# Kernel tuning notes

Hardware: AMD Instinct MI355X
Metric: run time of the kernel (lower is better)

## Reference

```python
import jax, jax.numpy as jnp
import numpy as np

STRIDE = 16
A = 9
PRE_NMS_TOP_N = 6000
POST_NMS_TOP_N = 300
NMS_THRESH = 0.7
MIN_SIZE = 16
H, W = 128, 192


def _generate_anchors(base_size=16, ratios=(0.5, 1.0, 2.0), scales=(8, 16, 32)):
    base = np.array([0, 0, base_size - 1, base_size - 1], dtype=np.float64)
    w = base[2] - base[0] + 1
    h = base[3] - base[1] + 1
    x_ctr = base[0] + 0.5 * (w - 1)
    y_ctr = base[1] + 0.5 * (h - 1)
    size = w * h
    ratios = np.array(ratios)
    ws = np.round(np.sqrt(size / ratios))
    hs = np.round(ws * ratios)
    ratio_anchors = np.stack([x_ctr - 0.5 * (ws - 1), y_ctr - 0.5 * (hs - 1),
                              x_ctr + 0.5 * (ws - 1), y_ctr + 0.5 * (hs - 1)], axis=1)
    out = []
    scales = np.array(scales)
    for a in ratio_anchors:
        aw = a[2] - a[0] + 1
        ah = a[3] - a[1] + 1
        xc = a[0] + 0.5 * (aw - 1)
        yc = a[1] + 0.5 * (ah - 1)
        ws2 = aw * scales
        hs2 = ah * scales
        out.append(np.stack([xc - 0.5 * (ws2 - 1), yc - 0.5 * (hs2 - 1),
                             xc + 0.5 * (ws2 - 1), yc + 0.5 * (hs2 - 1)], axis=1))
    return np.concatenate(out, axis=0).astype(np.float32)  # [9,4]


def setup_inputs() -> dict:
    key = jax.random.key(0)
    k1, k2 = jax.random.split(key)
    scores = jax.random.uniform(k1, (1, 2 * A, H, W), dtype=jnp.float32)
    bbox_deltas = 0.1 * jax.random.normal(k2, (1, 4 * A, H, W), dtype=jnp.float32)
    im_info = jnp.array([[H * STRIDE, W * STRIDE, 1.0]], dtype=jnp.float32)
    return {"scores": scores, "bbox_deltas": bbox_deltas, "im_info": im_info}


def _proposal_forward(scores, bbox_deltas, im_info):
    anchors_base = jnp.asarray(_generate_anchors())  # [A,4]
    sc = scores[:, A:, :, :]                          # fg scores [1,A,H,W]
    h, w = sc.shape[-2], sc.shape[-1]
    shift_x = (jnp.arange(w) * STRIDE).astype(sc.dtype)
    shift_y = (jnp.arange(h) * STRIDE).astype(sc.dtype)
    sy, sx = jnp.meshgrid(shift_y, shift_x, indexing='ij')
    shifts = jnp.stack([sx.ravel(), sy.ravel(), sx.ravel(), sy.ravel()], axis=1)  # [K,4]
    anchors = (anchors_base[None, :, :] + shifts[:, None, :]).reshape(-1, 4)      # [K*A,4]

    deltas = bbox_deltas.transpose(0, 2, 3, 1).reshape(-1, 4)
    deltas = jnp.concatenate([deltas[:, :2], jnp.clip(deltas[:, 2:], -10.0, 10.0)], axis=1)
    sc = sc.transpose(0, 2, 3, 1).reshape(-1)  # [K*A]

    widths = anchors[:, 2] - anchors[:, 0] + 1.0
    heights = anchors[:, 3] - anchors[:, 1] + 1.0
    ctr_x = anchors[:, 0] + 0.5 * widths
    ctr_y = anchors[:, 1] + 0.5 * heights
    dx, dy, dw, dh = deltas[:, 0], deltas[:, 1], deltas[:, 2], deltas[:, 3]
    pcx = dx * widths + ctr_x
    pcy = dy * heights + ctr_y
    pw = jnp.exp(dw) * widths
    ph = jnp.exp(dh) * heights
    x1 = pcx - 0.5 * pw
    y1 = pcy - 0.5 * ph
    x2 = pcx + 0.5 * pw
    y2 = pcy + 0.5 * ph

    info = im_info[0]
    x1 = jnp.clip(x1, 0.0, info[1] - 1.0)
    x2 = jnp.clip(x2, 0.0, info[1] - 1.0)
    y1 = jnp.clip(y1, 0.0, info[0] - 1.0)
    y2 = jnp.clip(y2, 0.0, info[0] - 1.0)
    proposals = jnp.stack([x1, y1, x2, y2], axis=1)

    # filter_boxes: mask (instead of dropping) boxes smaller than min_size*scale
    min_sz = MIN_SIZE * info[2]
    valid = ((x2 - x1 + 1.0) >= min_sz) & ((y2 - y1 + 1.0) >= min_sz)
    masked = jnp.where(valid, sc, -jnp.inf)

    # sort desc + pre_nms_topN
    top_scores, top_idx = jax.lax.top_k(masked, PRE_NMS_TOP_N)
    boxes = proposals[top_idx]               # [PRE,4], score-descending
    tvalid = top_scores > -jnp.inf

    # pairwise IoU (torchvision convention)
    area = (boxes[:, 2] - boxes[:, 0]) * (boxes[:, 3] - boxes[:, 1])
    lt = jnp.maximum(boxes[:, None, :2], boxes[None, :, :2])
    rb = jnp.minimum(boxes[:, None, 2:], boxes[None, :, 2:])
    wh = jnp.clip(rb - lt, 0.0)
    inter = wh[..., 0] * wh[..., 1]
    iou = inter / (area[:, None] + area[None, :] - inter)  # [PRE,PRE]

    # greedy NMS over score-sorted boxes
    n = PRE_NMS_TOP_N
    def step(keep, x):
        iou_col, v, i = x
        suppressed = jnp.any(keep & (iou_col > NMS_THRESH))
        k = v & jnp.logical_not(suppressed)
        keep = keep.at[i].set(k)
        return keep, k
    keep, _ = jax.lax.scan(step, jnp.zeros((n,), dtype=bool),
                           (iou.T, tvalid, jnp.arange(n)))

    # kept boxes first (stable => score order preserved), take post_nms_topN
    order = jnp.argsort(jnp.logical_not(keep).astype(jnp.int32), stable=True)[:POST_NMS_TOP_N]
    kept = keep[order]
    out_boxes = jnp.where(kept[:, None], boxes[order], 0.0)
    output = jnp.concatenate(
        [jnp.zeros((POST_NMS_TOP_N, 1), out_boxes.dtype), out_boxes], axis=1)
    return output  # [POST,5]: (batch_idx=0, x1,y1,x2,y2); rows beyond kept count are zero


def reference(scores, bbox_deltas, im_info):
    return _proposal_forward(scores, bbox_deltas, im_info)
```

## Files before the change

### kernel.cpp

```cpp
#include <hip/hip_runtime.h>

#define N_ANCH 221184
#define HW     24576
#define Wd     192
#define AA     9
#define TOPN   6000
#define POSTN  300
#define CAND_CAP 8192
#define NWORDS 94
#define NCHUNK 47
#define NBUCK  32768
#define BSHIFT 17

typedef unsigned long long u64;

__device__ const float c_aw[9] = {184.f,368.f,736.f,128.f,256.f,512.f, 88.f,176.f,352.f};
__device__ const float c_ah[9] = { 96.f,192.f,384.f,128.f,256.f,512.f,176.f,352.f,704.f};

__device__ __forceinline__ unsigned int rot15(unsigned int b) {
    return ((b << 7) | (b >> 8)) & 0x7FFFu;
}

__device__ __forceinline__ float4 decode_box(int a, int cell,
                                             const float* __restrict__ deltas,
                                             float info0, float info1, float info2,
                                             bool* valid) {
    int h = cell / Wd;
    int w = cell - h * Wd;
    const float* db = deltas + (size_t)(4 * a) * HW + cell;
    float dx = db[0];
    float dy = db[HW];
    float dw = db[2 * HW];
    float dh = db[3 * HW];
    dw = fminf(fmaxf(dw, -10.f), 10.f);
    dh = fminf(fmaxf(dh, -10.f), 10.f);

    float ww = c_aw[a], hh = c_ah[a];
    float cx = 16.f * (float)w + 8.f;
    float cy = 16.f * (float)h + 8.f;

    float pcx = __fadd_rn(__fmul_rn(dx, ww), cx);
    float pcy = __fadd_rn(__fmul_rn(dy, hh), cy);
    float pw  = __fmul_rn(expf(dw), ww);
    float ph  = __fmul_rn(expf(dh), hh);
    float hpw = __fmul_rn(0.5f, pw);
    float hph = __fmul_rn(0.5f, ph);
    float x1 = __fsub_rn(pcx, hpw);
    float x2 = __fadd_rn(pcx, hpw);
    float y1 = __fsub_rn(pcy, hph);
    float y2 = __fadd_rn(pcy, hph);

    float xmax = __fsub_rn(info1, 1.f);
    float ymax = __fsub_rn(info0, 1.f);
    x1 = fminf(fmaxf(x1, 0.f), xmax);
    x2 = fminf(fmaxf(x2, 0.f), xmax);
    y1 = fminf(fmaxf(y1, 0.f), ymax);
    y2 = fminf(fmaxf(y2, 0.f), ymax);

    float msz = __fmul_rn(16.f, info2);
    *valid = (__fadd_rn(__fsub_rn(x2, x1), 1.f) >= msz) &&
             (__fadd_rn(__fsub_rn(y2, y1), 1.f) >= msz);
    return make_float4(x1, y1, x2, y2);
}

__global__ __launch_bounds__(256) void init_kernel(float4* zH) {
    int t = blockIdx.x * 256 + threadIdx.x;
    zH[t] = make_float4(0.f, 0.f, 0.f, 0.f);
}

__global__ __launch_bounds__(256) void decode_kernel(const float* __restrict__ scores,
                                                     const float* __restrict__ deltas,
                                                     const float* __restrict__ iminfo,
                                                     unsigned int* __restrict__ keys,
                                                     unsigned int* __restrict__ hist,
                                                     float4* __restrict__ zA,
                                                     float4* __restrict__ zB) {
    __shared__ unsigned int lhp[NBUCK / 2];
    for (int i = threadIdx.x; i < NBUCK / 2; i += 256) lhp[i] = 0u;

    int t = blockIdx.x * 256 + threadIdx.x;
    float4 z = make_float4(0.f, 0.f, 0.f, 0.f);
    if (t < 4100) zA[t] = z;
    else if (t < 4148) zB[t - 4100] = z;

    int a = t / HW;
    int cell = t - a * HW;
    float score = scores[(AA + a) * HW + cell];
    bool valid;
    (void)decode_box(a, cell, deltas, iminfo[0], iminfo[1], iminfo[2], &valid);
    unsigned int sb = __float_as_uint(score);
    unsigned int key = valid ? ((sb & 0x80000000u) ? ~sb : (sb | 0x80000000u))
                             : 0x007FFFFFu;
    keys[t] = key;
    __syncthreads();
    unsigned int b = key >> BSHIFT;
    atomicAdd(&lhp[b >> 1], 1u << ((b & 1u) << 4));
    __syncthreads();
    for (int i = threadIdx.x; i < NBUCK / 2; i += 256) {
        unsigned int v = lhp[i];
        if (v) {
            unsigned int lo = v & 0xFFFFu, hi = v >> 16;
            if (lo) atomicAdd(&hist[rot15(2u * i)], lo);
            if (hi) atomicAdd(&hist[rot15(2u * i + 1u)], hi);
        }
    }
}

__global__ __launch_bounds__(256) void compact_kernel(const unsigned int* __restrict__ keys,
                                                      const unsigned int* __restrict__ hist,
                                                      unsigned int* __restrict__ state,
                                                      u64* __restrict__ cand) {
    __shared__ unsigned int sfx[256];
    __shared__ unsigned int sC, sGt, sT;
    int t = threadIdx.x;

    unsigned int part = 0;
    int rbase = t * 128;
    for (int j = 0; j < 128; ++j) part += hist[rot15((unsigned int)(rbase + j))];
    sfx[t] = part;
    __syncthreads();
    for (int d = 1; d < 256; d <<= 1) {
        unsigned int v = (t + d < 256) ? sfx[t + d] : 0u;
        __syncthreads();
        sfx[t] += v;
        __syncthreads();
    }
    {
        unsigned int ge = sfx[t];
        unsigned int gt = (t < 255) ? sfx[t + 1] : 0u;
        if (ge >= TOPN && gt < TOPN) { sC = (unsigned int)t; sGt = gt; }
    }
    __syncthreads();
    unsigned int cbase = sC * 128u;
    unsigned int gtA = sGt;
    unsigned int e = (t < 128) ? hist[rot15(cbase + (unsigned int)t)] : 0u;
    __syncthreads();
    sfx[t] = e;
    __syncthreads();
    for (int d = 1; d < 256; d <<= 1) {
        unsigned int v = (t + d < 256) ? sfx[t + d] : 0u;
        __syncthreads();
        sfx[t] += v;
        __syncthreads();
    }
    {
        unsigned int ge = sfx[t] + gtA;
        unsigned int gt = ((t < 255) ? sfx[t + 1] : 0u) + gtA;
        if (t < 128 && ge >= TOPN && gt < TOPN)
            sT = (cbase + (unsigned int)t) << BSHIFT;
    }
    __syncthreads();
    unsigned int T = sT;

    int i = blockIdx.x * 256 + t;
    unsigned int k = keys[i];
    if (k >= T) {
        unsigned int pos = atomicAdd(&state[2], 1u);
        if (pos < CAND_CAP) {
            int a = i / HW;
            int cell = i - a * HW;
            unsigned int aidx = (unsigned int)(cell * 9 + a);
            cand[pos] = ((u64)k << 32) | (u64)(~aidx);
        }
    }
}

__global__ __launch_bounds__(256) void rank_scatter_kernel(const u64* __restrict__ cand,
                                                           const float* __restrict__ deltas,
                                                           const float* __restrict__ iminfo,
                                                           float4* __restrict__ tb,
                                                           u64* __restrict__ vmask) {
    __shared__ u64 s[CAND_CAP];
    for (int j = threadIdx.x; j < CAND_CAP; j += 256) s[j] = cand[j];
    int part = threadIdx.x & 7;
    int i = blockIdx.x * 32 + (threadIdx.x >> 3);
    u64 k = cand[i];
    __syncthreads();
    const ulonglong2* sv = (const ulonglong2*)s;
    unsigned int cnt = 0;
    #pragma unroll 8
    for (int jj = part; jj < CAND_CAP / 2; jj += 8) {
        ulonglong2 v = sv[jj];
        cnt += (v.x > k) ? 1u : 0u;
        cnt += (v.y > k) ? 1u : 0u;
    }
    cnt += __shfl_xor(cnt, 1);
    cnt += __shfl_xor(cnt, 2);
    cnt += __shfl_xor(cnt, 4);
    if (part == 0 && k != 0ull && cnt < TOPN) {
        unsigned int aidx = ~((unsigned int)k);
        int a = (int)(aidx % 9u);
        int cell = (int)(aidx / 9u);
        bool valid;
        float4 box = decode_box(a, cell, deltas, iminfo[0], iminfo[1], iminfo[2], &valid);
        tb[cnt] = box;
        if ((unsigned int)(k >> 32) != 0x007FFFFFu)
            atomicOr(&vmask[cnt >> 6], 1ull << (cnt & 63));
    }
}

__global__ __launch_bounds__(64) void nms_matrix_kernel(const float4* __restrict__ tb,
                                                        u64* __restrict__ mat) {
    if (blockIdx.x < blockIdx.y) return;
    __shared__ float4 cb[64];
    int t = threadIdx.x;
    int c0 = blockIdx.x * 64;
    int col = c0 + t;
    cb[t] = (col < TOPN) ? tb[col] : make_float4(0.f, 0.f, 0.f, 0.f);
    __syncthreads();
    int row = blockIdx.y * 64 + t;
    if (row >= TOPN) return;
    float4 rb = tb[row];
    float rA = (rb.z - rb.x) * (rb.w - rb.y);
    u64 mask = 0ull;
    for (int c = 0; c < 64; ++c) {
        if (c0 + c >= TOPN) break;
        float4 b = cb[c];
        float lx = fmaxf(rb.x, b.x), ly = fmaxf(rb.y, b.y);
        float rx = fminf(rb.z, b.z), ry = fminf(rb.w, b.w);
        float iw = fmaxf(rx - lx, 0.f), ih = fmaxf(ry - ly, 0.f);
        float inter = iw * ih;
        float bA = (b.z - b.x) * (b.w - b.y);
        float iou = inter / ((rA + bA) - inter);
        if (iou > 0.7f) mask |= (1ull << c);
    }
    mat[(size_t)row * NWORDS + blockIdx.x] = mask;
}

__device__ __forceinline__ u64 rdl64(u64 v, int l) {
    unsigned int lo = (unsigned int)__builtin_amdgcn_readlane((int)(unsigned int)v, l);
    unsigned int hi = (unsigned int)__builtin_amdgcn_readlane((int)(unsigned int)(v >> 32), l);
    return ((u64)hi << 32) | (u64)lo;
}

__global__ __launch_bounds__(64) void nms_scan_kernel(const u64* __restrict__ mat,
                                                      const u64* __restrict__ vmask,
                                                      const float4* __restrict__ tb,
                                                      float* __restrict__ out) {
    int lane = threadIdx.x;
    u64 r0 = ~vmask[lane];
    u64 r1 = (lane < NWORDS - 64) ? ~vmask[64 + lane] : ~0ull;
    __shared__ int kept[POSTN];
    int cnt = 0;

    u64 a0, a1, b0, b1;
    {
        ulonglong2 vA = *(const ulonglong2*)(mat + (size_t)lane * NWORDS);
        ulonglong2 vB = *(const ulonglong2*)(mat + (size_t)(64 + lane) * NWORDS);
        a0 = vA.x; a1 = vA.y; b0 = vB.x; b1 = vB.y;
    }
    for (int c = 0; c < NCHUNK; ++c) {
        u64 na0 = 0, na1 = 0, nb0 = 0, nb1 = 0;
        if (c + 1 < NCHUNK) {
            const u64* pA = mat + (size_t)((c + 1) * 128 + lane) * NWORDS + 2 * (c + 1);
            const u64* pB = mat + (size_t)((c + 1) * 128 + 64 + lane) * NWORDS + 2 * (c + 1);
            ulonglong2 vA = *(const ulonglong2*)pA;
            ulonglong2 vB = *(const ulonglong2*)pB;
            na0 = vA.x; na1 = vA.y; nb0 = vB.x; nb1 = vB.y;
        }
        int w2 = 2 * c;
        u64 s0 = (w2 < 64) ? rdl64(r0, w2) : rdl64(r1, w2 - 64);
        u64 s1 = (w2 + 1 < 64) ? rdl64(r0, w2 + 1) : rdl64(r1, w2 + 1 - 64);
        if ((s0 & s1) != ~0ull) {
            int base = c * 128;
            u64 rem0 = s0, rem1 = s1, k0 = 0ull, k1 = 0ull;
            while (cnt < POSTN) {
                int b;
                if (~rem0) b = __ffsll((u64)~rem0) - 1;
                else if (~rem1) b = 64 + __ffsll((u64)~rem1) - 1;
                else break;
                if (lane == 0) kept[cnt] = base + b;
                ++cnt;
                u64 w0, w1;
                if (b < 64) {
                    w0 = rdl64(a0, b); w1 = rdl64(a1, b);
                    k0 |= 1ull << b; rem0 |= 1ull << b;
                } else {
                    int bb = b - 64;
                    w0 = rdl64(b0, bb); w1 = rdl64(b1, bb);
                    k1 |= 1ull << bb; rem1 |= 1ull << bb;
                }
                rem0 |= w0; rem1 |= w1;
            }
            if (cnt >= POSTN) break;
            u64 f0 = 0ull, f1 = 0ull, m0 = k0, m1 = k1;
            while (m0 | m1) {
                int idxs[8];
                #pragma unroll
                for (int j = 0; j < 8; ++j) {
                    int b = -1;
                    if (m0) { b = __ffsll(m0) - 1; m0 &= m0 - 1; }
                    else if (m1) { b = 64 + __ffsll(m1) - 1; m1 &= m1 - 1; }
                    idxs[j] = b;
                }
                u64 v0[8], v1[8];
                #pragma unroll
                for (int j = 0; j < 8; ++j) {
                    v0[j] = 0ull; v1[j] = 0ull;
                    if (idxs[j] >= 0) {
                        const u64* row = mat + (size_t)(base + idxs[j]) * NWORDS;
                        v0[j] = row[lane];
                        if (lane < NWORDS - 64) v1[j] = row[64 + lane];
                    }
                }
                #pragma unroll
                for (int j = 0; j < 8; ++j) { f0 |= v0[j]; f1 |= v1[j]; }
            }
            r0 |= f0; r1 |= f1;
        }
        a0 = na0; a1 = na1; b0 = nb0; b1 = nb1;
    }

    for (int r = lane; r < POSTN; r += 64) {
        float4 b = make_float4(0.f, 0.f, 0.f, 0.f);
        if (r < cnt) b = tb[kept[r]];
        float* o = out + r * 5;
        o[0] = 0.f; o[1] = b.x; o[2] = b.y; o[3] = b.z; o[4] = b.w;
    }
}

extern "C" void kernel_launch(void* const* d_in, const int* in_sizes, int n_in,
                              void* d_out, int out_size, void* d_ws, size_t ws_size,
                              hipStream_t stream) {
    const float* scores = (const float*)d_in[0];
    const float* deltas = (const float*)d_in[1];
    const float* iminfo = (const float*)d_in[2];
    float* out = (float*)d_out;

    char* ws = (char*)d_ws;
    unsigned int* keys    = (unsigned int*)(ws + 0);
    unsigned int* state   = (unsigned int*)(ws + 885760);
    u64*          cand    = (u64*)(ws + 885824);
    float4*       tb      = (float4*)(ws + 951360);
    u64*          vmask   = (u64*)(ws + 1047616);
    u64*          mat     = (u64*)(ws + 1048384);
    unsigned int* hist32k = (unsigned int*)(ws + 1048384);

    const int NB = N_ANCH / 256;

    init_kernel<<<32, 256, 0, stream>>>((float4*)hist32k);
    decode_kernel<<<NB, 256, 0, stream>>>(scores, deltas, iminfo, keys, hist32k,
                                          (float4*)(ws + 885760),
                                          (float4*)vmask);
    compact_kernel<<<NB, 256, 0, stream>>>(keys, hist32k, state, cand);
    rank_scatter_kernel<<<CAND_CAP / 32, 256, 0, stream>>>(cand, deltas, iminfo, tb, vmask);
    nms_matrix_kernel<<<dim3(NWORDS, NWORDS), 64, 0, stream>>>(tb, mat);
    nms_scan_kernel<<<1, 64, 0, stream>>>(mat, vmask, tb, out);
}
```

Measured before the change: 240.5 us.

## Transpose histogram layout for coalesced prefix reads and pack NMS diagonal blocks

```diff
diff --git a/kernel.cpp b/kernel.cpp
--- a/kernel.cpp
+++ b/kernel.cpp
@@ -17,8 +17,8 @@
 __device__ const float c_aw[9] = {184.f,368.f,736.f,128.f,256.f,512.f, 88.f,176.f,352.f};
 __device__ const float c_ah[9] = { 96.f,192.f,384.f,128.f,256.f,512.f,176.f,352.f,704.f};
 
-__device__ __forceinline__ unsigned int rot15(unsigned int b) {
-    return ((b << 7) | (b >> 8)) & 0x7FFFu;
+__device__ __forceinline__ unsigned int s15(unsigned int b) {
+    return ((b & 0x7Fu) << 8) | (b >> 7);
 }
 
 __device__ __forceinline__ float4 decode_box(int a, int cell,
@@ -100,8 +100,8 @@
         unsigned int v = lhp[i];
         if (v) {
             unsigned int lo = v & 0xFFFFu, hi = v >> 16;
-            if (lo) atomicAdd(&hist[rot15(2u * i)], lo);
-            if (hi) atomicAdd(&hist[rot15(2u * i + 1u)], hi);
+            if (lo) atomicAdd(&hist[s15(2u * i)], lo);
+            if (hi) atomicAdd(&hist[s15(2u * i + 1u)], hi);
         }
     }
 }
@@ -115,8 +115,7 @@
     int t = threadIdx.x;
 
     unsigned int part = 0;
-    int rbase = t * 128;
-    for (int j = 0; j < 128; ++j) part += hist[rot15((unsigned int)(rbase + j))];
+    for (int iter = 0; iter < 128; ++iter) part += hist[iter * 256 + t];
     sfx[t] = part;
     __syncthreads();
     for (int d = 1; d < 256; d <<= 1) {
@@ -131,9 +130,9 @@
         if (ge >= TOPN && gt < TOPN) { sC = (unsigned int)t; sGt = gt; }
     }
     __syncthreads();
-    unsigned int cbase = sC * 128u;
+    unsigned int C = sC;
     unsigned int gtA = sGt;
-    unsigned int e = (t < 128) ? hist[rot15(cbase + (unsigned int)t)] : 0u;
+    unsigned int e = (t < 128) ? hist[((unsigned int)t << 8) | C] : 0u;
     __syncthreads();
     sfx[t] = e;
     __syncthreads();
@@ -147,7 +146,7 @@
         unsigned int ge = sfx[t] + gtA;
         unsigned int gt = ((t < 255) ? sfx[t + 1] : 0u) + gtA;
         if (t < 128 && ge >= TOPN && gt < TOPN)
-            sT = (cbase + (unsigned int)t) << BSHIFT;
+            sT = (C * 128u + (unsigned int)t) << BSHIFT;
     }
     __syncthreads();
     unsigned int T = sT;
@@ -200,7 +199,8 @@
 }
 
 __global__ __launch_bounds__(64) void nms_matrix_kernel(const float4* __restrict__ tb,
-                                                        u64* __restrict__ mat) {
+                                                        u64* __restrict__ mat,
+                                                        u64* __restrict__ diagp) {
     if (blockIdx.x < blockIdx.y) return;
     __shared__ float4 cb[64];
     int t = threadIdx.x;
@@ -225,6 +225,11 @@
         if (iou > 0.7f) mask |= (1ull << c);
     }
     mat[(size_t)row * NWORDS + blockIdx.x] = mask;
+    if ((blockIdx.x >> 1) == (blockIdx.y >> 1)) {
+        int c = blockIdx.x >> 1;
+        int rin = ((blockIdx.y & 1) << 6) + t;
+        diagp[((size_t)c * 128 + rin) * 2 + (blockIdx.x & 1)] = mask;
+    }
 }
 
 __device__ __forceinline__ u64 rdl64(u64 v, int l) {
@@ -234,6 +239,7 @@
 }
 
 __global__ __launch_bounds__(64) void nms_scan_kernel(const u64* __restrict__ mat,
+                                                      const u64* __restrict__ diagp,
                                                       const u64* __restrict__ vmask,
                                                       const float4* __restrict__ tb,
                                                       float* __restrict__ out) {
@@ -243,19 +249,18 @@
     __shared__ int kept[POSTN];
     int cnt = 0;
 
+    const ulonglong2* dp = (const ulonglong2*)diagp;
     u64 a0, a1, b0, b1;
     {
-        ulonglong2 vA = *(const ulonglong2*)(mat + (size_t)lane * NWORDS);
-        ulonglong2 vB = *(const ulonglong2*)(mat + (size_t)(64 + lane) * NWORDS);
+        ulonglong2 vA = dp[lane];
+        ulonglong2 vB = dp[64 + lane];
         a0 = vA.x; a1 = vA.y; b0 = vB.x; b1 = vB.y;
     }
     for (int c = 0; c < NCHUNK; ++c) {
         u64 na0 = 0, na1 = 0, nb0 = 0, nb1 = 0;
         if (c + 1 < NCHUNK) {
-            const u64* pA = mat + (size_t)((c + 1) * 128 + lane) * NWORDS + 2 * (c + 1);
-            const u64* pB = mat + (size_t)((c + 1) * 128 + 64 + lane) * NWORDS + 2 * (c + 1);
-            ulonglong2 vA = *(const ulonglong2*)pA;
-            ulonglong2 vB = *(const ulonglong2*)pB;
+            ulonglong2 vA = dp[(c + 1) * 128 + lane];
+            ulonglong2 vB = dp[(c + 1) * 128 + 64 + lane];
             na0 = vA.x; na1 = vA.y; nb0 = vB.x; nb1 = vB.y;
         }
         int w2 = 2 * c;
@@ -335,15 +340,15 @@
     u64*          vmask   = (u64*)(ws + 1047616);
     u64*          mat     = (u64*)(ws + 1048384);
     unsigned int* hist32k = (unsigned int*)(ws + 1048384);
+    u64*          diagp   = (u64*)(ws + 0);
 
     const int NB = N_ANCH / 256;
 
     init_kernel<<<32, 256, 0, stream>>>((float4*)hist32k);
     decode_kernel<<<NB, 256, 0, stream>>>(scores, deltas, iminfo, keys, hist32k,
-                                          (float4*)(ws + 885760),
-                                          (float4*)vmask);
+                                          (float4*)(ws + 885760), (float4*)vmask);
     compact_kernel<<<NB, 256, 0, stream>>>(keys, hist32k, state, cand);
     rank_scatter_kernel<<<CAND_CAP / 32, 256, 0, stream>>>(cand, deltas, iminfo, tb, vmask);
-    nms_matrix_kernel<<<dim3(NWORDS, NWORDS), 64, 0, stream>>>(tb, mat);
-    nms_scan_kernel<<<1, 64, 0, stream>>>(mat, vmask, tb, out);
-}
+    nms_matrix_kernel<<<dim3(NWORDS, NWORDS), 64, 0, stream>>>(tb, mat, diagp);
+    nms_scan_kernel<<<1, 64, 0, stream>>>(mat, diagp, vmask, tb, out);
+}
```

Result: no change. 241.0 us (+0.2%).
